# Optimization experiments

Measured on AMD Instinct MI355X. Metric: run time of the kernel, lower is better.

Reference implementation:

```python
import jax, jax.numpy as jnp
import numpy as np

# ---- static problem configuration (mirrors Barrier_Net param) ----
B, NN, NO, SD = 100000, 16, 8, 4        # agents, neighbors, obstacles, state dim
H, PHI_OUT, ADIM = 64, 16, 2            # MLP hidden, deepset latent, action dim
DS, B_GAMMA, B_EXPH = 0.2, 0.01, 1.0    # r_safe, barrier gain, barrier exponent
PHI_MIN, PHI_MAX = -1.0, 1.0            # empty-action range
A_MIN, A_MAX = -2.0, 2.0                # final action range
D_OBS = 1 + (NN + 1) * SD + 2 * NO      # 85


def mlp2(x, w1, b1, w2, b2):
    return jax.nn.relu(x @ w1 + b1) @ w2 + b2


def setup_inputs() -> dict:
    key = jax.random.key(0)
    ks = jax.random.split(key, 10)
    x = jax.random.normal(ks[0], (B, D_OBS), jnp.float32)
    x = x.at[:, 0].set(float(NN))  # first entry encodes the neighbor count

    def w(k, shape):
        return jax.random.normal(k, shape, jnp.float32) * 0.1

    return {
        "x": x,
        "phi_w1": w(ks[1], (SD, H)), "phi_b1": jnp.zeros((H,), jnp.float32),
        "phi_w2": w(ks[2], (H, PHI_OUT)), "phi_b2": jnp.zeros((PHI_OUT,), jnp.float32),
        "obs_w1": w(ks[3], (2, H)), "obs_b1": jnp.zeros((H,), jnp.float32),
        "obs_w2": w(ks[4], (H, PHI_OUT)), "obs_b2": jnp.zeros((PHI_OUT,), jnp.float32),
        "rho_w1": w(ks[5], (PHI_OUT, H)), "rho_b1": jnp.zeros((H,), jnp.float32),
        "rho_w2": w(ks[6], (H, ADIM)), "rho_b2": jnp.zeros((ADIM,), jnp.float32),
        "psi_w1": w(ks[7], (ADIM + 2, H)), "psi_b1": jnp.zeros((H,), jnp.float32),
        "psi_w2": w(ks[8], (H, ADIM)), "psi_b2": jnp.zeros((ADIM,), jnp.float32),
    }


def reference(x, phi_w1, phi_b1, phi_w2, phi_b2, obs_w1, obs_b1, obs_w2, obs_b2,
              rho_w1, rho_b1, rho_w2, rho_b2, psi_w1, psi_b1, psi_w2, psi_b2):
    # observation layout: [nn, self(SD), nn relative neighbor states(SD each), no obstacles(2 each)]
    nb = x[:, 1 + SD:1 + SD + NN * SD].reshape(B, NN, SD)   # relative neighbor states
    ob = x[:, 1 + (NN + 1) * SD:].reshape(B, NO, 2)          # relative obstacle positions

    # --- DeepSet: permutation-invariant sum of phi over elements, then rho ---
    phi_sum = mlp2(nb, phi_w1, phi_b1, phi_w2, phi_b2).sum(axis=1)   # [B, PHI_OUT]
    obs_sum = mlp2(ob, obs_w1, obs_b1, obs_w2, obs_b2).sum(axis=1)   # [B, PHI_OUT]
    rho = mlp2(phi_sum + obs_sum, rho_w1, rho_b1, rho_w2, rho_b2)    # [B, ADIM]

    # --- empty(): psi head on cat(rho, g) with tanh range squash to [phi_min, phi_max] ---
    g = x[:, 0:2]
    e = mlp2(jnp.concatenate([rho, g], axis=1), psi_w1, psi_b1, psi_w2, psi_b2)
    empty = (jnp.tanh(e) + 1.0) * 0.5 * (PHI_MAX - PHI_MIN) + PHI_MIN

    # --- barrier: gather neighbor rel-positions, scalar potential, scatter-add per agent ---
    p_ij = -nb[..., 0:2]                                    # [B, NN, 2], p^i - p^j
    h_ij = jnp.linalg.norm(p_ij, axis=-1) - DS              # [B, NN]
    barrier = jnp.sum((B_GAMMA / h_ij ** B_EXPH)[..., None] * p_ij, axis=1)  # [B, 2]

    action = jnp.tanh(empty + barrier)
    return (action + 1.0) * 0.5 * (A_MAX - A_MIN) + A_MIN
```

## Files before the change

kernel.cpp:

```cpp
#include <hip/hip_runtime.h>

#define BATCH 100000

typedef float v2 __attribute__((ext_vector_type(2)));

__device__ __forceinline__ v2 fma2(v2 a, v2 b, v2 c) { return __builtin_elementwise_fma(a, b, c); }
__device__ __forceinline__ v2 relu2(v2 a) { v2 z = {0.f, 0.f}; return __builtin_elementwise_max(a, z); }
__device__ __forceinline__ v2 splat(float a) { v2 r = {a, a}; return r; }
__device__ __forceinline__ v2 ldv2(const float* p) { return *(const v2*)p; }

__global__ __launch_bounds__(256, 4) void barrier_net(
    const float* __restrict__ x,
    const float* __restrict__ phi_w1, const float* __restrict__ phi_b1,
    const float* __restrict__ phi_w2, const float* __restrict__ phi_b2,
    const float* __restrict__ obs_w1, const float* __restrict__ obs_b1,
    const float* __restrict__ obs_w2, const float* __restrict__ obs_b2,
    const float* __restrict__ rho_w1, const float* __restrict__ rho_b1,
    const float* __restrict__ rho_w2, const float* __restrict__ rho_b2,
    const float* __restrict__ psi_w1, const float* __restrict__ psi_b1,
    const float* __restrict__ psi_w2, const float* __restrict__ psi_b2,
    float2* __restrict__ out)
{
    const int tid = blockIdx.x * 256 + threadIdx.x;
    const int s = tid >> 1;
    const int t = tid & 1;
    if (s >= BATCH) return;
    const float* xr = x + (size_t)s * 85;

    float nb[8][4];
    const int nbase = 5 + 32 * t;
#pragma unroll
    for (int n = 0; n < 8; ++n)
#pragma unroll
        for (int k = 0; k < 4; ++k)
            nb[n][k] = xr[nbase + 4 * n + k];

    float ob[4][2];
    const int obase = 69 + 8 * t;
#pragma unroll
    for (int o = 0; o < 4; ++o) {
        ob[o][0] = xr[obase + 2 * o];
        ob[o][1] = xr[obase + 2 * o + 1];
    }

    const float g0 = xr[0], g1 = xr[1];

    float bar0 = 0.f, bar1 = 0.f;
#pragma unroll
    for (int n = 0; n < 8; ++n) {
        float p0 = -nb[n][0], p1 = -nb[n][1];
        float r  = __builtin_amdgcn_sqrtf(fmaf(p0, p0, p1 * p1));
        float sc = 0.01f * __builtin_amdgcn_rcpf(r - 0.2f);
        bar0 = fmaf(sc, p0, bar0);
        bar1 = fmaf(sc, p1, bar1);
    }

    v2 acc[8];
#pragma unroll
    for (int p = 0; p < 8; ++p)
        acc[p] = fma2(splat(8.f), ldv2(phi_b2 + 2 * p),
                 fma2(splat(4.f), ldv2(obs_b2 + 2 * p), splat(0.f)));

#pragma unroll 2
    for (int c = 0; c < 8; ++c) {
        const int hb = c * 8;
        v2 hsv[4] = {{0.f,0.f},{0.f,0.f},{0.f,0.f},{0.f,0.f}};
#pragma unroll
        for (int n = 0; n < 8; ++n) {
#pragma unroll
            for (int p = 0; p < 4; ++p) {
                v2 tv = fma2(splat(nb[n][0]), ldv2(phi_w1 + hb + 2 * p),
                        fma2(splat(nb[n][1]), ldv2(phi_w1 + 64 + hb + 2 * p),
                        fma2(splat(nb[n][2]), ldv2(phi_w1 + 128 + hb + 2 * p),
                        fma2(splat(nb[n][3]), ldv2(phi_w1 + 192 + hb + 2 * p),
                                              ldv2(phi_b1 + hb + 2 * p)))));
                hsv[p] += relu2(tv);
            }
        }
#pragma unroll
        for (int p = 0; p < 4; ++p) {
            const float* r0 = phi_w2 + (size_t)(hb + 2 * p) * 16;
            v2 hx = splat(hsv[p].x), hy = splat(hsv[p].y);
#pragma unroll
            for (int q = 0; q < 8; ++q)
                acc[q] = fma2(hy, ldv2(r0 + 16 + 2 * q),
                         fma2(hx, ldv2(r0 + 2 * q), acc[q]));
        }
    }

#pragma unroll 2
    for (int c = 0; c < 8; ++c) {
        const int hb = c * 8;
        v2 hsv[4] = {{0.f,0.f},{0.f,0.f},{0.f,0.f},{0.f,0.f}};
#pragma unroll
        for (int o = 0; o < 4; ++o) {
#pragma unroll
            for (int p = 0; p < 4; ++p) {
                v2 tv = fma2(splat(ob[o][0]), ldv2(obs_w1 + hb + 2 * p),
                        fma2(splat(ob[o][1]), ldv2(obs_w1 + 64 + hb + 2 * p),
                                              ldv2(obs_b1 + hb + 2 * p)));
                hsv[p] += relu2(tv);
            }
        }
#pragma unroll
        for (int p = 0; p < 4; ++p) {
            const float* r0 = obs_w2 + (size_t)(hb + 2 * p) * 16;
            v2 hx = splat(hsv[p].x), hy = splat(hsv[p].y);
#pragma unroll
            for (int q = 0; q < 8; ++q)
                acc[q] = fma2(hy, ldv2(r0 + 16 + 2 * q),
                         fma2(hx, ldv2(r0 + 2 * q), acc[q]));
        }
    }

#pragma unroll
    for (int p = 0; p < 8; ++p) {
        acc[p].x += __shfl_xor(acc[p].x, 1);
        acc[p].y += __shfl_xor(acc[p].y, 1);
    }
    bar0 += __shfl_xor(bar0, 1);
    bar1 += __shfl_xor(bar1, 1);

    v2 rr = ldv2(rho_b2);
#pragma unroll 2
    for (int c = 0; c < 8; ++c) {
        const int hb = c * 8;
        v2 tt[4];
#pragma unroll
        for (int p = 0; p < 4; ++p)
            tt[p] = ldv2(rho_b1 + hb + 2 * p);
#pragma unroll
        for (int j = 0; j < 8; ++j) {
            v2 ax = splat(acc[j].x), ay = splat(acc[j].y);
            const float* rj0 = rho_w1 + (size_t)(2 * j) * 64 + hb;
            const float* rj1 = rho_w1 + (size_t)(2 * j + 1) * 64 + hb;
#pragma unroll
            for (int p = 0; p < 4; ++p)
                tt[p] = fma2(ay, ldv2(rj1 + 2 * p),
                        fma2(ax, ldv2(rj0 + 2 * p), tt[p]));
        }
#pragma unroll
        for (int p = 0; p < 4; ++p) {
            v2 u = relu2(tt[p]);
            rr = fma2(splat(u.x), ldv2(rho_w2 + 2 * (hb + 2 * p)), rr);
            rr = fma2(splat(u.y), ldv2(rho_w2 + 2 * (hb + 2 * p) + 2), rr);
        }
    }

    v2 ee = ldv2(psi_b2);
#pragma unroll 2
    for (int c = 0; c < 8; ++c) {
        const int hb = c * 8;
#pragma unroll
        for (int p = 0; p < 4; ++p) {
            v2 tv = fma2(splat(rr.x), ldv2(psi_w1 + hb + 2 * p),
                    fma2(splat(rr.y), ldv2(psi_w1 + 64 + hb + 2 * p),
                    fma2(splat(g0),   ldv2(psi_w1 + 128 + hb + 2 * p),
                    fma2(splat(g1),   ldv2(psi_w1 + 192 + hb + 2 * p),
                                      ldv2(psi_b1 + hb + 2 * p)))));
            v2 u = relu2(tv);
            ee = fma2(splat(u.x), ldv2(psi_w2 + 2 * (hb + 2 * p)), ee);
            ee = fma2(splat(u.y), ldv2(psi_w2 + 2 * (hb + 2 * p) + 2), ee);
        }
    }

    if (t == 0) {
        float a0 = tanhf(tanhf(ee.x) + bar0);
        float a1 = tanhf(tanhf(ee.y) + bar1);
        out[s] = make_float2(2.f * a0, 2.f * a1);
    }
}

extern "C" void kernel_launch(void* const* d_in, const int* in_sizes, int n_in,
                              void* d_out, int out_size, void* d_ws, size_t ws_size,
                              hipStream_t stream) {
    const int threads = BATCH * 2;
    dim3 grid((threads + 255) / 256), block(256);
    barrier_net<<<grid, block, 0, stream>>>(
        (const float*)d_in[0],
        (const float*)d_in[1],  (const float*)d_in[2],  (const float*)d_in[3],  (const float*)d_in[4],
        (const float*)d_in[5],  (const float*)d_in[6],  (const float*)d_in[7],  (const float*)d_in[8],
        (const float*)d_in[9],  (const float*)d_in[10], (const float*)d_in[11], (const float*)d_in[12],
        (const float*)d_in[13], (const float*)d_in[14], (const float*)d_in[15], (const float*)d_in[16],
        (float2*)d_out);
}
```

Baseline: 145.4 us.

## Process two samples per thread pair to amortize weight loads

Each thread pair now handles two agents instead of one, so every weight value loaded for the phi/obs/rho/psi MLPs is reused across two samples' arithmetic. The grid is halved and launch bounds relaxed to one block per CU to give the compiler more registers. This is meant to cut the scalar/vector weight-load overhead per FMA, at the cost of higher register pressure and lower occupancy, and fewer waves to hide the strided input loads.

```diff
diff --git a/kernel.cpp b/kernel.cpp
--- a/kernel.cpp
+++ b/kernel.cpp
@@ -9,7 +9,7 @@
 __device__ __forceinline__ v2 splat(float a) { v2 r = {a, a}; return r; }
 __device__ __forceinline__ v2 ldv2(const float* p) { return *(const v2*)p; }
 
-__global__ __launch_bounds__(256, 4) void barrier_net(
+__global__ __launch_bounds__(256, 1) void barrier_net(
     const float* __restrict__ x,
     const float* __restrict__ phi_w1, const float* __restrict__ phi_b1,
     const float* __restrict__ phi_w2, const float* __restrict__ phi_b2,
@@ -22,161 +22,196 @@
     float2* __restrict__ out)
 {
     const int tid = blockIdx.x * 256 + threadIdx.x;
-    const int s = tid >> 1;
-    const int t = tid & 1;
-    if (s >= BATCH) return;
-    const float* xr = x + (size_t)s * 85;
-
-    float nb[8][4];
+    const int pr = tid >> 1;
+    const int t  = tid & 1;
+    const int s0 = 2 * pr;
+    const int s1 = 2 * pr + 1;
+    if (s0 >= BATCH) return;
+    const float* xr[2];
+    xr[0] = x + (size_t)s0 * 85;
+    xr[1] = x + (size_t)(s1 < BATCH ? s1 : s0) * 85;
+
+    float nb[2][8][4];
     const int nbase = 5 + 32 * t;
 #pragma unroll
-    for (int n = 0; n < 8; ++n)
-#pragma unroll
-        for (int k = 0; k < 4; ++k)
-            nb[n][k] = xr[nbase + 4 * n + k];
-
-    float ob[4][2];
+    for (int u = 0; u < 2; ++u)
+#pragma unroll
+        for (int n = 0; n < 8; ++n)
+#pragma unroll
+            for (int k = 0; k < 4; ++k)
+                nb[u][n][k] = xr[u][nbase + 4 * n + k];
+
+    float ob[2][4][2];
     const int obase = 69 + 8 * t;
 #pragma unroll
-    for (int o = 0; o < 4; ++o) {
-        ob[o][0] = xr[obase + 2 * o];
-        ob[o][1] = xr[obase + 2 * o + 1];
-    }
-
-    const float g0 = xr[0], g1 = xr[1];
-
-    float bar0 = 0.f, bar1 = 0.f;
-#pragma unroll
-    for (int n = 0; n < 8; ++n) {
-        float p0 = -nb[n][0], p1 = -nb[n][1];
-        float r  = __builtin_amdgcn_sqrtf(fmaf(p0, p0, p1 * p1));
-        float sc = 0.01f * __builtin_amdgcn_rcpf(r - 0.2f);
-        bar0 = fmaf(sc, p0, bar0);
-        bar1 = fmaf(sc, p1, bar1);
-    }
-
-    v2 acc[8];
-#pragma unroll
-    for (int p = 0; p < 8; ++p)
-        acc[p] = fma2(splat(8.f), ldv2(phi_b2 + 2 * p),
-                 fma2(splat(4.f), ldv2(obs_b2 + 2 * p), splat(0.f)));
-
-#pragma unroll 2
-    for (int c = 0; c < 8; ++c) {
-        const int hb = c * 8;
-        v2 hsv[4] = {{0.f,0.f},{0.f,0.f},{0.f,0.f},{0.f,0.f}};
+    for (int u = 0; u < 2; ++u)
+#pragma unroll
+        for (int o = 0; o < 4; ++o) {
+            ob[u][o][0] = xr[u][obase + 2 * o];
+            ob[u][o][1] = xr[u][obase + 2 * o + 1];
+        }
+
+    float g0[2], g1[2];
+#pragma unroll
+    for (int u = 0; u < 2; ++u) { g0[u] = xr[u][0]; g1[u] = xr[u][1]; }
+
+    float bar0[2] = {0.f, 0.f}, bar1[2] = {0.f, 0.f};
+#pragma unroll
+    for (int u = 0; u < 2; ++u)
 #pragma unroll
         for (int n = 0; n < 8; ++n) {
-#pragma unroll
-            for (int p = 0; p < 4; ++p) {
-                v2 tv = fma2(splat(nb[n][0]), ldv2(phi_w1 + hb + 2 * p),
-                        fma2(splat(nb[n][1]), ldv2(phi_w1 + 64 + hb + 2 * p),
-                        fma2(splat(nb[n][2]), ldv2(phi_w1 + 128 + hb + 2 * p),
-                        fma2(splat(nb[n][3]), ldv2(phi_w1 + 192 + hb + 2 * p),
-                                              ldv2(phi_b1 + hb + 2 * p)))));
-                hsv[p] += relu2(tv);
-            }
-        }
-#pragma unroll
-        for (int p = 0; p < 4; ++p) {
-            const float* r0 = phi_w2 + (size_t)(hb + 2 * p) * 16;
-            v2 hx = splat(hsv[p].x), hy = splat(hsv[p].y);
-#pragma unroll
-            for (int q = 0; q < 8; ++q)
-                acc[q] = fma2(hy, ldv2(r0 + 16 + 2 * q),
-                         fma2(hx, ldv2(r0 + 2 * q), acc[q]));
-        }
-    }
-
-#pragma unroll 2
-    for (int c = 0; c < 8; ++c) {
-        const int hb = c * 8;
-        v2 hsv[4] = {{0.f,0.f},{0.f,0.f},{0.f,0.f},{0.f,0.f}};
-#pragma unroll
-        for (int o = 0; o < 4; ++o) {
-#pragma unroll
-            for (int p = 0; p < 4; ++p) {
-                v2 tv = fma2(splat(ob[o][0]), ldv2(obs_w1 + hb + 2 * p),
-                        fma2(splat(ob[o][1]), ldv2(obs_w1 + 64 + hb + 2 * p),
-                                              ldv2(obs_b1 + hb + 2 * p)));
-                hsv[p] += relu2(tv);
-            }
-        }
-#pragma unroll
-        for (int p = 0; p < 4; ++p) {
-            const float* r0 = obs_w2 + (size_t)(hb + 2 * p) * 16;
-            v2 hx = splat(hsv[p].x), hy = splat(hsv[p].y);
-#pragma unroll
-            for (int q = 0; q < 8; ++q)
-                acc[q] = fma2(hy, ldv2(r0 + 16 + 2 * q),
-                         fma2(hx, ldv2(r0 + 2 * q), acc[q]));
-        }
-    }
-
+            float p0 = -nb[u][n][0], p1 = -nb[u][n][1];
+            float r  = __builtin_amdgcn_sqrtf(fmaf(p0, p0, p1 * p1));
+            float sc = 0.01f * __builtin_amdgcn_rcpf(r - 0.2f);
+            bar0[u] = fmaf(sc, p0, bar0[u]);
+            bar1[u] = fmaf(sc, p1, bar1[u]);
+        }
+
+    v2 acc[2][8];
 #pragma unroll
     for (int p = 0; p < 8; ++p) {
-        acc[p].x += __shfl_xor(acc[p].x, 1);
-        acc[p].y += __shfl_xor(acc[p].y, 1);
-    }
-    bar0 += __shfl_xor(bar0, 1);
-    bar1 += __shfl_xor(bar1, 1);
-
-    v2 rr = ldv2(rho_b2);
-#pragma unroll 2
-    for (int c = 0; c < 8; ++c) {
-        const int hb = c * 8;
-        v2 tt[4];
-#pragma unroll
-        for (int p = 0; p < 4; ++p)
-            tt[p] = ldv2(rho_b1 + hb + 2 * p);
-#pragma unroll
-        for (int j = 0; j < 8; ++j) {
-            v2 ax = splat(acc[j].x), ay = splat(acc[j].y);
-            const float* rj0 = rho_w1 + (size_t)(2 * j) * 64 + hb;
-            const float* rj1 = rho_w1 + (size_t)(2 * j + 1) * 64 + hb;
+        v2 b = fma2(splat(8.f), ldv2(phi_b2 + 2 * p),
+               fma2(splat(4.f), ldv2(obs_b2 + 2 * p), splat(0.f)));
+        acc[0][p] = b; acc[1][p] = b;
+    }
+
+#pragma unroll 2
+    for (int c = 0; c < 8; ++c) {
+        const int hb = c * 8;
+#pragma unroll
+        for (int u = 0; u < 2; ++u) {
+            v2 hsv[4] = {{0.f,0.f},{0.f,0.f},{0.f,0.f},{0.f,0.f}};
+#pragma unroll
+            for (int n = 0; n < 8; ++n) {
+#pragma unroll
+                for (int p = 0; p < 4; ++p) {
+                    v2 tv = fma2(splat(nb[u][n][0]), ldv2(phi_w1 + hb + 2 * p),
+                            fma2(splat(nb[u][n][1]), ldv2(phi_w1 + 64 + hb + 2 * p),
+                            fma2(splat(nb[u][n][2]), ldv2(phi_w1 + 128 + hb + 2 * p),
+                            fma2(splat(nb[u][n][3]), ldv2(phi_w1 + 192 + hb + 2 * p),
+                                                     ldv2(phi_b1 + hb + 2 * p)))));
+                    hsv[p] += relu2(tv);
+                }
+            }
+#pragma unroll
+            for (int p = 0; p < 4; ++p) {
+                const float* r0 = phi_w2 + (size_t)(hb + 2 * p) * 16;
+                v2 hx = splat(hsv[p].x), hy = splat(hsv[p].y);
+#pragma unroll
+                for (int q = 0; q < 8; ++q)
+                    acc[u][q] = fma2(hy, ldv2(r0 + 16 + 2 * q),
+                                fma2(hx, ldv2(r0 + 2 * q), acc[u][q]));
+            }
+        }
+    }
+
+#pragma unroll 2
+    for (int c = 0; c < 8; ++c) {
+        const int hb = c * 8;
+#pragma unroll
+        for (int u = 0; u < 2; ++u) {
+            v2 hsv[4] = {{0.f,0.f},{0.f,0.f},{0.f,0.f},{0.f,0.f}};
+#pragma unroll
+            for (int o = 0; o < 4; ++o) {
+#pragma unroll
+                for (int p = 0; p < 4; ++p) {
+                    v2 tv = fma2(splat(ob[u][o][0]), ldv2(obs_w1 + hb + 2 * p),
+                            fma2(splat(ob[u][o][1]), ldv2(obs_w1 + 64 + hb + 2 * p),
+                                                     ldv2(obs_b1 + hb + 2 * p)));
+                    hsv[p] += relu2(tv);
+                }
+            }
+#pragma unroll
+            for (int p = 0; p < 4; ++p) {
+                const float* r0 = obs_w2 + (size_t)(hb + 2 * p) * 16;
+                v2 hx = splat(hsv[p].x), hy = splat(hsv[p].y);
+#pragma unroll
+                for (int q = 0; q < 8; ++q)
+                    acc[u][q] = fma2(hy, ldv2(r0 + 16 + 2 * q),
+                                fma2(hx, ldv2(r0 + 2 * q), acc[u][q]));
+            }
+        }
+    }
+
+#pragma unroll
+    for (int u = 0; u < 2; ++u) {
+#pragma unroll
+        for (int p = 0; p < 8; ++p) {
+            acc[u][p].x += __shfl_xor(acc[u][p].x, 1);
+            acc[u][p].y += __shfl_xor(acc[u][p].y, 1);
+        }
+        bar0[u] += __shfl_xor(bar0[u], 1);
+        bar1[u] += __shfl_xor(bar1[u], 1);
+    }
+
+    v2 rr[2];
+    rr[0] = ldv2(rho_b2); rr[1] = rr[0];
+#pragma unroll 2
+    for (int c = 0; c < 8; ++c) {
+        const int hb = c * 8;
+#pragma unroll
+        for (int u = 0; u < 2; ++u) {
+            v2 tt[4];
 #pragma unroll
             for (int p = 0; p < 4; ++p)
-                tt[p] = fma2(ay, ldv2(rj1 + 2 * p),
-                        fma2(ax, ldv2(rj0 + 2 * p), tt[p]));
-        }
-#pragma unroll
-        for (int p = 0; p < 4; ++p) {
-            v2 u = relu2(tt[p]);
-            rr = fma2(splat(u.x), ldv2(rho_w2 + 2 * (hb + 2 * p)), rr);
-            rr = fma2(splat(u.y), ldv2(rho_w2 + 2 * (hb + 2 * p) + 2), rr);
-        }
-    }
-
-    v2 ee = ldv2(psi_b2);
-#pragma unroll 2
-    for (int c = 0; c < 8; ++c) {
-        const int hb = c * 8;
-#pragma unroll
-        for (int p = 0; p < 4; ++p) {
-            v2 tv = fma2(splat(rr.x), ldv2(psi_w1 + hb + 2 * p),
-                    fma2(splat(rr.y), ldv2(psi_w1 + 64 + hb + 2 * p),
-                    fma2(splat(g0),   ldv2(psi_w1 + 128 + hb + 2 * p),
-                    fma2(splat(g1),   ldv2(psi_w1 + 192 + hb + 2 * p),
-                                      ldv2(psi_b1 + hb + 2 * p)))));
-            v2 u = relu2(tv);
-            ee = fma2(splat(u.x), ldv2(psi_w2 + 2 * (hb + 2 * p)), ee);
-            ee = fma2(splat(u.y), ldv2(psi_w2 + 2 * (hb + 2 * p) + 2), ee);
+                tt[p] = ldv2(rho_b1 + hb + 2 * p);
+#pragma unroll
+            for (int j = 0; j < 8; ++j) {
+                v2 ax = splat(acc[u][j].x), ay = splat(acc[u][j].y);
+                const float* rj0 = rho_w1 + (size_t)(2 * j) * 64 + hb;
+                const float* rj1 = rho_w1 + (size_t)(2 * j + 1) * 64 + hb;
+#pragma unroll
+                for (int p = 0; p < 4; ++p)
+                    tt[p] = fma2(ay, ldv2(rj1 + 2 * p),
+                            fma2(ax, ldv2(rj0 + 2 * p), tt[p]));
+            }
+#pragma unroll
+            for (int p = 0; p < 4; ++p) {
+                v2 w = relu2(tt[p]);
+                rr[u] = fma2(splat(w.x), ldv2(rho_w2 + 2 * (hb + 2 * p)), rr[u]);
+                rr[u] = fma2(splat(w.y), ldv2(rho_w2 + 2 * (hb + 2 * p) + 2), rr[u]);
+            }
+        }
+    }
+
+    v2 ee[2];
+    ee[0] = ldv2(psi_b2); ee[1] = ee[0];
+#pragma unroll 2
+    for (int c = 0; c < 8; ++c) {
+        const int hb = c * 8;
+#pragma unroll
+        for (int u = 0; u < 2; ++u) {
+#pragma unroll
+            for (int p = 0; p < 4; ++p) {
+                v2 tv = fma2(splat(rr[u].x), ldv2(psi_w1 + hb + 2 * p),
+                        fma2(splat(rr[u].y), ldv2(psi_w1 + 64 + hb + 2 * p),
+                        fma2(splat(g0[u]),   ldv2(psi_w1 + 128 + hb + 2 * p),
+                        fma2(splat(g1[u]),   ldv2(psi_w1 + 192 + hb + 2 * p),
+                                             ldv2(psi_b1 + hb + 2 * p)))));
+                v2 w = relu2(tv);
+                ee[u] = fma2(splat(w.x), ldv2(psi_w2 + 2 * (hb + 2 * p)), ee[u]);
+                ee[u] = fma2(splat(w.y), ldv2(psi_w2 + 2 * (hb + 2 * p) + 2), ee[u]);
+            }
         }
     }
 
     if (t == 0) {
-        float a0 = tanhf(tanhf(ee.x) + bar0);
-        float a1 = tanhf(tanhf(ee.y) + bar1);
-        out[s] = make_float2(2.f * a0, 2.f * a1);
+        float a00 = tanhf(tanhf(ee[0].x) + bar0[0]);
+        float a01 = tanhf(tanhf(ee[0].y) + bar1[0]);
+        out[s0] = make_float2(2.f * a00, 2.f * a01);
+        if (s1 < BATCH) {
+            float a10 = tanhf(tanhf(ee[1].x) + bar0[1]);
+            float a11 = tanhf(tanhf(ee[1].y) + bar1[1]);
+            out[s1] = make_float2(2.f * a10, 2.f * a11);
+        }
     }
 }
 
 extern "C" void kernel_launch(void* const* d_in, const int* in_sizes, int n_in,
                               void* d_out, int out_size, void* d_ws, size_t ws_size,
                               hipStream_t stream) {
-    const int threads = BATCH * 2;
-    dim3 grid((threads + 255) / 256), block(256);
-    barrier_net<<<grid, block, 0, stream>>>(
+    const int blocks = (BATCH + 255) / 256;
+    barrier_net<<<blocks, 256, 0, stream>>>(
         (const float*)d_in[0],
         (const float*)d_in[1],  (const float*)d_in[2],  (const float*)d_in[3],  (const float*)d_in[4],
         (const float*)d_in[5],  (const float*)d_in[6],  (const float*)d_in[7],  (const float*)d_in[8],
```

Result: slower. 189.1 us (+30.0%).
